# Kernel tuning notes

Measured on AMD Instinct MI355X. Metric: run time of the kernel, lower is better.

## Reference

```python
import jax, jax.numpy as jnp
import numpy as np

HEADS = 8
DIM_HEAD = 64
QUERY_DIM = 512
INNER = HEADS * DIM_HEAD
DIAG_OFFSET = 1
T_TEMP = 1.0
NEG_INF = -1e9  # used via -inf below; kept for clarity


def setup_inputs() -> dict:
    key = jax.random.key(0)
    ks = jax.random.split(key, 8)
    b, s, f = 2, 2048, 16
    x = jax.random.normal(ks[0], (b, s, f, QUERY_DIM), dtype=jnp.float32)
    pos_bias = jax.random.normal(ks[1], (HEADS, f, f), dtype=jnp.float32)
    w_scale = 0.02
    Wq = jax.random.normal(ks[2], (QUERY_DIM, INNER), dtype=jnp.float32) * w_scale
    Wk = jax.random.normal(ks[3], (QUERY_DIM, INNER), dtype=jnp.float32) * w_scale
    Wv = jax.random.normal(ks[4], (QUERY_DIM, INNER), dtype=jnp.float32) * w_scale
    Wo = jax.random.normal(ks[5], (INNER, QUERY_DIM), dtype=jnp.float32) * w_scale
    bo = jax.random.normal(ks[6], (QUERY_DIM,), dtype=jnp.float32) * w_scale
    return {"x": x, "pos_bias": pos_bias, "Wq": Wq, "Wk": Wk, "Wv": Wv, "Wo": Wo, "bo": bo}


def reference(x, pos_bias, Wq, Wk, Wv, Wo, bo):
    # x: [b, s, f, c] -- temporal attention over the frame axis f per spatial token
    b, s, f, _ = x.shape
    scale = DIM_HEAD ** -0.5
    q = (x @ Wq).reshape(b, s, f, HEADS, DIM_HEAD)
    k = (x @ Wk).reshape(b, s, f, HEADS, DIM_HEAD)
    v = (x @ Wv).reshape(b, s, f, HEADS, DIM_HEAD)
    # scores over frames: [b, s, h, f_q, f_k]
    w = jnp.einsum('bsihd,bsjhd->bshij', q * scale, k)
    w = w + pos_bias[None, None]  # [h, f, f] relative position bias
    # attend_prev_only causal mask (strict, diag_offset=1)
    causal = jnp.triu(jnp.ones((f, f), dtype=jnp.float32), k=DIAG_OFFSET)
    w = w + jnp.where(causal == 1.0, -jnp.inf, 0.0)
    # faithful to source: subtract row max, then softmax with temperature
    w = w - jax.lax.stop_gradient(jnp.max(w, axis=-1, keepdims=True))
    p = jax.nn.softmax(w.astype(jnp.float32) / T_TEMP, axis=-1).astype(w.dtype)
    out = jnp.einsum('bshij,bsjhd->bsihd', p, v).reshape(b, s, f, INNER)
    return out @ Wo + bo
```

## Files before the change

kernel.cpp:

```cpp
#include <hip/hip_runtime.h>

typedef unsigned short u16;
typedef __attribute__((ext_vector_type(8))) unsigned short u16x8;
typedef __attribute__((ext_vector_type(8))) __bf16 bf16x8;
typedef __attribute__((ext_vector_type(4))) float f32x4;

#define M_ROWS 65536
#define NQKV   1536
#define KDIM   512

typedef __attribute__((address_space(1))) const void gconst_void;
typedef __attribute__((address_space(3))) void lds_void;

static __device__ __forceinline__ u16 f2bf(float f) {
  unsigned u = __builtin_bit_cast(unsigned, f);
  u += 0x7FFFu + ((u >> 16) & 1u);
  return (u16)(u >> 16);
}

static __device__ __forceinline__ f32x4 mfma_bf16(u16x8 a, u16x8 b, f32x4 c) {
  return __builtin_amdgcn_mfma_f32_16x16x32_bf16(
      __builtin_bit_cast(bf16x8, a), __builtin_bit_cast(bf16x8, b), c, 0, 0, 0);
}

__global__ void conv_x(const float* __restrict__ x, u16* __restrict__ xb) {
  const size_t t = (size_t)blockIdx.x * 256 + threadIdx.x;
  f32x4 a = *(const f32x4*)(x + t * 8);
  f32x4 b = *(const f32x4*)(x + t * 8 + 4);
  u16x8 w;
#pragma unroll
  for (int e = 0; e < 4; ++e) { w[e] = f2bf(a[e]); w[e + 4] = f2bf(b[e]); }
  *(u16x8*)(xb + t * 8) = w;
}

__global__ void convW_qkv_t(const float* __restrict__ Wq, const float* __restrict__ Wk,
                            const float* __restrict__ Wv, u16* __restrict__ Wt) {
  __shared__ float tile[32][33];
  const int bn = blockIdx.x * 32;
  const int bk = blockIdx.y * 32;
  const int tx = threadIdx.x & 31, ty = threadIdx.x >> 5;
  const float* W = (bn < 512) ? Wq : ((bn < 1024) ? Wk : Wv);
  const int coln = bn & 511;
#pragma unroll
  for (int r = 0; r < 32; r += 8)
    tile[ty + r][tx] = W[(size_t)(bk + ty + r) * 512 + coln + tx];
  __syncthreads();
#pragma unroll
  for (int r = 0; r < 32; r += 8)
    Wt[(size_t)(bn + ty + r) * 512 + bk + tx] = f2bf(tile[tx][ty + r]);
}

__global__ void convWo_t(const float* __restrict__ Wo, u16* __restrict__ Wt) {
  __shared__ float tile[32][33];
  const int bn = blockIdx.x * 32;
  const int bk = blockIdx.y * 32;
  const int tx = threadIdx.x & 31, ty = threadIdx.x >> 5;
#pragma unroll
  for (int r = 0; r < 32; r += 8)
    tile[ty + r][tx] = Wo[(size_t)(bk + ty + r) * 512 + bn + tx];
  __syncthreads();
#pragma unroll
  for (int r = 0; r < 32; r += 8)
    Wt[(size_t)(bn + ty + r) * 512 + bk + tx] = f2bf(tile[tx][ty + r]);
}

__global__ __launch_bounds__(512, 2)
void gemm_qkv_attn(const u16* __restrict__ A, const u16* __restrict__ Wt,
                   const float* __restrict__ pos_bias, u16* __restrict__ attnbuf) {
  __shared__ __attribute__((aligned(16))) u16 smem[57344];
  u16* Ab   = smem;
  u16* Bb   = smem + 32768;
  u16* qkvT = smem;
  u16* Pl   = smem + 51200;

  const int tid  = threadIdx.x;
  const int lane = tid & 63;
  const int wid  = tid >> 6;
  const int wm   = wid >> 1;
  const int wn   = wid & 1;
  const int lg   = lane >> 4;
  const int lc   = lane & 15;
  const int srow = lane >> 3;
  const int sg   = (lane & 7) ^ srow;

  const int nwg  = gridDim.x;
  const int cpx  = nwg >> 3;
  const int flat = blockIdx.x;
  const int swz  = (flat & 7) * cpx + (flat >> 3);
  const int mt   = swz >> 3;
  const int h    = swz & 7;
  const int row0 = mt * 256;

  auto stagePh = [&](int ph, int b, int kt) {
    const int k0 = kt * 64;
    if (ph < 2) {
#pragma unroll
      for (int cc = 0; cc < 2; ++cc) {
        const int rl = wid * 32 + (ph * 2 + cc) * 8;
        const u16* src = A + (size_t)(row0 + rl + srow) * KDIM + k0 + sg * 8;
        __builtin_amdgcn_global_load_lds((gconst_void*)src,
                                         (lds_void*)&Ab[b * 16384 + rl * 64], 16, 0, 0);
      }
    } else {
      const int nj = (ph == 2) ? 2 : 1;
#pragma unroll
      for (int jj = 0; jj < 2; ++jj) {
        if (jj < nj) {
          const int j  = (ph == 2) ? jj : 2;
          const int rl = wid * 24 + j * 8;
          const int n  = rl + srow;
          const int grow = (n >> 6) * 512 + h * 64 + (n & 63);
          const u16* src = Wt + (size_t)grow * KDIM + k0 + sg * 8;
          __builtin_amdgcn_global_load_lds((gconst_void*)src,
                                           (lds_void*)&Bb[b * 12288 + rl * 64], 16, 0, 0);
        }
      }
    }
  };

  f32x4 acc[4][6];
#pragma unroll
  for (int mi = 0; mi < 4; ++mi)
#pragma unroll
    for (int ni = 0; ni < 6; ++ni) acc[mi][ni] = (f32x4){0.f, 0.f, 0.f, 0.f};

#pragma unroll
  for (int ph = 0; ph < 4; ++ph) stagePh(ph, 0, 0);
  asm volatile("s_waitcnt vmcnt(0)" ::: "memory");
  __builtin_amdgcn_s_barrier();

  for (int t = 0; t < 8; ++t) {
    const int  c   = t & 1;
    const bool pre = (t + 1) < 8;
    const u16* Asb = &Ab[c * 16384];
    const u16* Bsb = &Bb[c * 12288];
    u16x8 af[2], bfr[6];

#pragma unroll
    for (int ph = 0; ph < 4; ++ph) {
      const int ks = ph >> 1;
      const int mh = ph & 1;
      const int gsw = ((ks * 4 + lg) ^ (lc & 7)) << 3;
      if (mh == 0) {
#pragma unroll
        for (int ni = 0; ni < 6; ++ni)
          bfr[ni] = *(const u16x8*)&Bsb[(wn * 96 + ni * 16 + lc) * 64 + gsw];
      }
#pragma unroll
      for (int i = 0; i < 2; ++i)
        af[i] = *(const u16x8*)&Asb[(wm * 64 + (mh * 2 + i) * 16 + lc) * 64 + gsw];
      if (pre) stagePh(ph, c ^ 1, t + 1);

      __builtin_amdgcn_s_barrier();
      asm volatile("s_waitcnt lgkmcnt(0)" ::: "memory");
      __builtin_amdgcn_sched_barrier(0);
      __builtin_amdgcn_s_setprio(1);
#pragma unroll
      for (int i = 0; i < 2; ++i)
#pragma unroll
        for (int ni = 0; ni < 6; ++ni)
          acc[mh * 2 + i][ni] = mfma_bf16(af[i], bfr[ni], acc[mh * 2 + i][ni]);
      __builtin_amdgcn_s_setprio(0);
      __builtin_amdgcn_sched_barrier(0);
      if (ph < 3) __builtin_amdgcn_s_barrier();
    }
    asm volatile("s_waitcnt vmcnt(0)" ::: "memory");
    __builtin_amdgcn_s_barrier();
  }

#pragma unroll
  for (int mi = 0; mi < 4; ++mi)
#pragma unroll
    for (int ni = 0; ni < 6; ++ni) {
      const int col = wn * 96 + ni * 16 + lc;
      const int rb  = wm * 64 + mi * 16 + lg * 4;
#pragma unroll
      for (int r = 0; r < 4; ++r)
        qkvT[(rb + r) * 200 + col] = f2bf(acc[mi][ni][r]);
    }
  __syncthreads();

  const float scale = 0.125f;
  const f32x4 zf = {0.f, 0.f, 0.f, 0.f};
#pragma unroll
  for (int tt = 0; tt < 2; ++tt) {
    const int tok = wid * 2 + tt;
    const int rb  = tok * 16;
    const int qb  = (rb + lc) * 200;

    u16x8 aq0 = *(const u16x8*)&qkvT[qb + 0  + lg * 8];
    u16x8 aq1 = *(const u16x8*)&qkvT[qb + 32 + lg * 8];
    u16x8 bk0 = *(const u16x8*)&qkvT[qb + 64 + lg * 8];
    u16x8 bk1 = *(const u16x8*)&qkvT[qb + 96 + lg * 8];
    f32x4 s = mfma_bf16(aq0, bk0, zf);
    s = mfma_bf16(aq1, bk1, s);

    const int pb = wid * 512 + tt * 256;
#pragma unroll
    for (int r = 0; r < 4; ++r) {
      const int i = lg * 4 + r;
      float sv = s[r] * scale + pos_bias[h * 256 + i * 16 + lc];
      if (lc > i) sv = -1e30f;
      float m = sv;
#pragma unroll
      for (int off = 8; off >= 1; off >>= 1) m = fmaxf(m, __shfl_xor(m, off));
      float e = __expf(sv - m);
      float sm = e;
#pragma unroll
      for (int off = 8; off >= 1; off >>= 1) sm += __shfl_xor(sm, off);
      Pl[pb + i * 16 + lc] = f2bf(e / sm);
    }
    asm volatile("s_waitcnt lgkmcnt(0)" ::: "memory");

    u16x8 ap = {0, 0, 0, 0, 0, 0, 0, 0};
    if (lane < 32) ap = *(const u16x8*)&Pl[pb + lc * 16 + lg * 8];

#pragma unroll
    for (int nd = 0; nd < 4; ++nd) {
      u16x8 bv = {0, 0, 0, 0, 0, 0, 0, 0};
      if (lane < 32) {
#pragma unroll
        for (int jj = 0; jj < 8; ++jj) {
          const int j = lg * 8 + jj;
          bv[jj] = qkvT[(rb + j) * 200 + 128 + nd * 16 + lc];
        }
      }
      f32x4 o = mfma_bf16(ap, bv, zf);
#pragma unroll
      for (int r = 0; r < 4; ++r) {
        const int i = lg * 4 + r;
        attnbuf[(size_t)(row0 + rb + i) * 512 + h * 64 + nd * 16 + lc] = f2bf(o[r]);
      }
    }
  }
}

template <bool CF32>
__global__ __launch_bounds__(512, 2)
void gemm256(const u16* __restrict__ A, const u16* __restrict__ Bt,
             void* __restrict__ Cp, const float* __restrict__ bias,
             int N, int K, int n_tiles) {
  __shared__ __attribute__((aligned(16))) u16 smem[4][256 * 64];

  const int tid  = threadIdx.x;
  const int lane = tid & 63;
  const int wid  = tid >> 6;
  const int wm   = wid >> 2;
  const int wn   = wid & 3;
  const int lg   = lane >> 4;
  const int lc   = lane & 15;
  const int srow = lane >> 3;
  const int sg   = (lane & 7) ^ srow;

  const int nwg  = gridDim.x;
  const int cpx  = nwg >> 3;
  const int flat = blockIdx.x;
  const int swz  = (flat & 7) * cpx + (flat >> 3);
  const int mt   = swz / n_tiles;
  const int nt   = swz % n_tiles;
  const int row0 = mt * 256, col0 = nt * 256;

  auto stagePh = [&](int ph, int b, int kt) {
    const int k0 = kt * 64;
#pragma unroll
    for (int cc = 0; cc < 2; ++cc) {
      if (ph < 2) {
        const int c2 = ph * 2 + cc;
        const int rl = wid * 32 + c2 * 8;
        const u16* src = A + (size_t)(row0 + rl + srow) * K + k0 + sg * 8;
        __builtin_amdgcn_global_load_lds((gconst_void*)src,
                                         (lds_void*)&smem[b][rl * 64], 16, 0, 0);
      } else {
        const int c2 = (ph - 2) * 2 + cc;
        const int rl = wid * 32 + c2 * 8;
        const u16* src = Bt + (size_t)(col0 + rl + srow) * K + k0 + sg * 8;
        __builtin_amdgcn_global_load_lds((gconst_void*)src,
                                         (lds_void*)&smem[2 + b][rl * 64], 16, 0, 0);
      }
    }
  };

  f32x4 acc[8][4];
#pragma unroll
  for (int mi = 0; mi < 8; ++mi)
#pragma unroll
    for (int ni = 0; ni < 4; ++ni) acc[mi][ni] = (f32x4){0.f, 0.f, 0.f, 0.f};

  const int nkt = K >> 6;

#pragma unroll
  for (int ph = 0; ph < 4; ++ph) stagePh(ph, 0, 0);
  asm volatile("s_waitcnt vmcnt(0)" ::: "memory");
  __builtin_amdgcn_s_barrier();

  for (int t = 0; t < nkt; ++t) {
    const int  c   = t & 1;
    const bool pre = (t + 1) < nkt;
    const u16* Asb = &smem[c][0];
    const u16* Bsb = &smem[2 + c][0];
    u16x8 af[4], bfr[4];

#pragma unroll
    for (int ph = 0; ph < 4; ++ph) {
      const int ks = ph >> 1;
      const int mh = ph & 1;
      const int gsw = ((ks * 4 + lg) ^ (lc & 7)) << 3;
      if (mh == 0) {
#pragma unroll
        for (int ni = 0; ni < 4; ++ni)
          bfr[ni] = *(const u16x8*)&Bsb[(wn * 64 + ni * 16 + lc) * 64 + gsw];
      }
#pragma unroll
      for (int i = 0; i < 4; ++i)
        af[i] = *(const u16x8*)&Asb[(wm * 128 + (mh * 4 + i) * 16 + lc) * 64 + gsw];
      if (pre) stagePh(ph, c ^ 1, t + 1);

      __builtin_amdgcn_s_barrier();
      asm volatile("s_waitcnt lgkmcnt(0)" ::: "memory");
      __builtin_amdgcn_sched_barrier(0);
      __builtin_amdgcn_s_setprio(1);
#pragma unroll
      for (int i = 0; i < 4; ++i)
#pragma unroll
        for (int ni = 0; ni < 4; ++ni)
          acc[mh * 4 + i][ni] = mfma_bf16(af[i], bfr[ni], acc[mh * 4 + i][ni]);
      __builtin_amdgcn_s_setprio(0);
      __builtin_amdgcn_sched_barrier(0);
      if (ph < 3) __builtin_amdgcn_s_barrier();
    }
    asm volatile("s_waitcnt vmcnt(0)" ::: "memory");
    __builtin_amdgcn_s_barrier();
  }

  const int gmb = row0 + wm * 128;
  const int gnb = col0 + wn * 64;
#pragma unroll
  for (int mi = 0; mi < 8; ++mi)
#pragma unroll
    for (int ni = 0; ni < 4; ++ni) {
      const int gm = gmb + mi * 16 + lg * 4;
      const int gn = gnb + ni * 16 + lc;
      f32x4 v = acc[mi][ni];
      if constexpr (CF32) {
        float* C = (float*)Cp;
        float bv = bias[gn];
#pragma unroll
        for (int r = 0; r < 4; ++r) C[(size_t)(gm + r) * N + gn] = v[r] + bv;
      } else {
        u16* C = (u16*)Cp;
#pragma unroll
        for (int r = 0; r < 4; ++r) C[(size_t)(gm + r) * N + gn] = f2bf(v[r]);
      }
    }
}

extern "C" void kernel_launch(void* const* d_in, const int* in_sizes, int n_in,
                              void* d_out, int out_size, void* d_ws, size_t ws_size,
                              hipStream_t stream) {
  const float* x        = (const float*)d_in[0];
  const float* pos_bias = (const float*)d_in[1];
  const float* Wq       = (const float*)d_in[2];
  const float* Wk       = (const float*)d_in[3];
  const float* Wv       = (const float*)d_in[4];
  const float* Wo       = (const float*)d_in[5];
  const float* bo       = (const float*)d_in[6];
  float* out            = (float*)d_out;

  u16* xb      = (u16*)d_ws;
  u16* attnbuf = xb + (size_t)M_ROWS * 512;
  u16* Wo_t    = attnbuf + (size_t)M_ROWS * 512;
  u16* Wqkv_t  = (u16*)d_out;

  conv_x<<<dim3(M_ROWS * KDIM / (256 * 8)), dim3(256), 0, stream>>>(x, xb);

  convW_qkv_t<<<dim3(48, 16), dim3(256), 0, stream>>>(Wq, Wk, Wv, Wqkv_t);

  gemm_qkv_attn<<<dim3(2048), dim3(512), 0, stream>>>(xb, Wqkv_t, pos_bias, attnbuf);

  convWo_t<<<dim3(16, 16), dim3(256), 0, stream>>>(Wo, Wo_t);

  gemm256<true><<<dim3(512), dim3(512), 0, stream>>>(
      attnbuf, Wo_t, (void*)out, bo, 512, KDIM, 2);
}
```

Before: 225.1 us.

## Triple-buffer A tiles with two-ahead prefetch and retile output GEMM

Both GEMM kernels now keep three LDS buffers for the A operand and two for B. A is prefetched two k-steps ahead and B one ahead, and the end-of-iteration vmcnt(0) drain is replaced by a partial vmcnt(4) wait before each step. This is meant to overlap global-to-LDS loads with MFMA work instead of stalling at every k-step. The output projection is also retiled from 256x256 to 256x128 blocks, doubling the grid to 1024 workgroups. LDS use in the fused QKV kernel grows, and correctness now depends on the vmcnt counts matching the exact load issue order.

```diff
diff --git a/kernel.cpp b/kernel.cpp
--- a/kernel.cpp
+++ b/kernel.cpp
@@ -6,8 +6,8 @@
 typedef __attribute__((ext_vector_type(4))) float f32x4;
 
 #define M_ROWS 65536
-#define NQKV   1536
 #define KDIM   512
+#define NKT    8
 
 typedef __attribute__((address_space(1))) const void gconst_void;
 typedef __attribute__((address_space(3))) void lds_void;
@@ -67,9 +67,9 @@
 __global__ __launch_bounds__(512, 2)
 void gemm_qkv_attn(const u16* __restrict__ A, const u16* __restrict__ Wt,
                    const float* __restrict__ pos_bias, u16* __restrict__ attnbuf) {
-  __shared__ __attribute__((aligned(16))) u16 smem[57344];
+  __shared__ __attribute__((aligned(16))) u16 smem[73728];
   u16* Ab   = smem;
-  u16* Bb   = smem + 32768;
+  u16* Bb   = smem + 49152;
   u16* qkvT = smem;
   u16* Pl   = smem + 51200;
 
@@ -91,32 +91,19 @@
   const int h    = swz & 7;
   const int row0 = mt * 256;
 
-  auto stagePh = [&](int ph, int b, int kt) {
-    const int k0 = kt * 64;
-    if (ph < 2) {
-#pragma unroll
-      for (int cc = 0; cc < 2; ++cc) {
-        const int rl = wid * 32 + (ph * 2 + cc) * 8;
-        const u16* src = A + (size_t)(row0 + rl + srow) * KDIM + k0 + sg * 8;
-        __builtin_amdgcn_global_load_lds((gconst_void*)src,
-                                         (lds_void*)&Ab[b * 16384 + rl * 64], 16, 0, 0);
-      }
-    } else {
-      const int nj = (ph == 2) ? 2 : 1;
-#pragma unroll
-      for (int jj = 0; jj < 2; ++jj) {
-        if (jj < nj) {
-          const int j  = (ph == 2) ? jj : 2;
-          const int rl = wid * 24 + j * 8;
-          const int n  = rl + srow;
-          const int grow = (n >> 6) * 512 + h * 64 + (n & 63);
-          const u16* src = Wt + (size_t)grow * KDIM + k0 + sg * 8;
-          __builtin_amdgcn_global_load_lds((gconst_void*)src,
-                                           (lds_void*)&Bb[b * 12288 + rl * 64], 16, 0, 0);
-        }
-      }
-    }
+  auto stageA = [&](int buf, int unit, int kt) {
+    const int rl = unit * 64 + wid * 8;
+    const u16* src = A + (size_t)(row0 + rl + srow) * KDIM + kt * 64 + sg * 8;
+    __builtin_amdgcn_global_load_lds((gconst_void*)src,
+                                     (lds_void*)&Ab[buf * 16384 + rl * 64], 16, 0, 0);
   };
+  auto stageB = [&](int buf, int unit, int kt) {
+    const int rl = unit * 64 + wid * 8;
+    const int grow = unit * 512 + h * 64 + wid * 8 + srow;
+    const u16* src = Wt + (size_t)grow * KDIM + kt * 64 + sg * 8;
+    __builtin_amdgcn_global_load_lds((gconst_void*)src,
+                                     (lds_void*)&Bb[buf * 12288 + rl * 64], 16, 0, 0);
+  };
 
   f32x4 acc[4][6];
 #pragma unroll
@@ -125,17 +112,24 @@
     for (int ni = 0; ni < 6; ++ni) acc[mi][ni] = (f32x4){0.f, 0.f, 0.f, 0.f};
 
 #pragma unroll
-  for (int ph = 0; ph < 4; ++ph) stagePh(ph, 0, 0);
-  asm volatile("s_waitcnt vmcnt(0)" ::: "memory");
-  __builtin_amdgcn_s_barrier();
-
-  for (int t = 0; t < 8; ++t) {
-    const int  c   = t & 1;
-    const bool pre = (t + 1) < 8;
-    const u16* Asb = &Ab[c * 16384];
-    const u16* Bsb = &Bb[c * 12288];
+  for (int u = 0; u < 4; ++u) stageA(0, u, 0);
+#pragma unroll
+  for (int u = 0; u < 3; ++u) stageB(0, u, 0);
+#pragma unroll
+  for (int u = 0; u < 4; ++u) stageA(1, u, 1);
+
+  for (int t = 0; t < NKT; ++t) {
+    const int  ab   = t % 3;
+    const int  bb   = t & 1;
+    const bool preB = (t + 1) < NKT;
+    const bool preA = (t + 2) < NKT;
+    const int  ab2  = (t + 2) % 3;
+
+    if (t < NKT - 1) asm volatile("s_waitcnt vmcnt(4)" ::: "memory");
+    else             asm volatile("s_waitcnt vmcnt(0)" ::: "memory");
+    __builtin_amdgcn_s_barrier();
+
     u16x8 af[2], bfr[6];
-
 #pragma unroll
     for (int ph = 0; ph < 4; ++ph) {
       const int ks = ph >> 1;
@@ -144,12 +138,16 @@
       if (mh == 0) {
 #pragma unroll
         for (int ni = 0; ni < 6; ++ni)
-          bfr[ni] = *(const u16x8*)&Bsb[(wn * 96 + ni * 16 + lc) * 64 + gsw];
+          bfr[ni] = *(const u16x8*)&Bb[bb * 12288 + (wn * 96 + ni * 16 + lc) * 64 + gsw];
       }
 #pragma unroll
       for (int i = 0; i < 2; ++i)
-        af[i] = *(const u16x8*)&Asb[(wm * 64 + (mh * 2 + i) * 16 + lc) * 64 + gsw];
-      if (pre) stagePh(ph, c ^ 1, t + 1);
+        af[i] = *(const u16x8*)&Ab[ab * 16384 + (wm * 64 + (mh * 2 + i) * 16 + lc) * 64 + gsw];
+
+      if (ph == 0 && preB) { stageB(bb ^ 1, 0, t + 1); stageB(bb ^ 1, 1, t + 1); }
+      if (ph == 1) { if (preB) stageB(bb ^ 1, 2, t + 1); if (preA) stageA(ab2, 0, t + 2); }
+      if (ph == 2 && preA) { stageA(ab2, 1, t + 2); stageA(ab2, 2, t + 2); }
+      if (ph == 3 && preA) { stageA(ab2, 3, t + 2); }
 
       __builtin_amdgcn_s_barrier();
       asm volatile("s_waitcnt lgkmcnt(0)" ::: "memory");
@@ -164,9 +162,8 @@
       __builtin_amdgcn_sched_barrier(0);
       if (ph < 3) __builtin_amdgcn_s_barrier();
     }
-    asm volatile("s_waitcnt vmcnt(0)" ::: "memory");
-    __builtin_amdgcn_s_barrier();
   }
+  __syncthreads();
 
 #pragma unroll
   for (int mi = 0; mi < 4; ++mi)
@@ -235,18 +232,18 @@
   }
 }
 
-template <bool CF32>
 __global__ __launch_bounds__(512, 2)
-void gemm256(const u16* __restrict__ A, const u16* __restrict__ Bt,
-             void* __restrict__ Cp, const float* __restrict__ bias,
-             int N, int K, int n_tiles) {
-  __shared__ __attribute__((aligned(16))) u16 smem[4][256 * 64];
+void gemm_out(const u16* __restrict__ A, const u16* __restrict__ Bt,
+              float* __restrict__ C, const float* __restrict__ bias) {
+  __shared__ __attribute__((aligned(16))) u16 smem[65536];
+  u16* Ab = smem;
+  u16* Bb = smem + 49152;
 
   const int tid  = threadIdx.x;
   const int lane = tid & 63;
   const int wid  = tid >> 6;
-  const int wm   = wid >> 2;
-  const int wn   = wid & 3;
+  const int wm   = wid >> 1;
+  const int wn   = wid & 1;
   const int lg   = lane >> 4;
   const int lc   = lane & 15;
   const int srow = lane >> 3;
@@ -256,50 +253,48 @@
   const int cpx  = nwg >> 3;
   const int flat = blockIdx.x;
   const int swz  = (flat & 7) * cpx + (flat >> 3);
-  const int mt   = swz / n_tiles;
-  const int nt   = swz % n_tiles;
-  const int row0 = mt * 256, col0 = nt * 256;
-
-  auto stagePh = [&](int ph, int b, int kt) {
-    const int k0 = kt * 64;
-#pragma unroll
-    for (int cc = 0; cc < 2; ++cc) {
-      if (ph < 2) {
-        const int c2 = ph * 2 + cc;
-        const int rl = wid * 32 + c2 * 8;
-        const u16* src = A + (size_t)(row0 + rl + srow) * K + k0 + sg * 8;
-        __builtin_amdgcn_global_load_lds((gconst_void*)src,
-                                         (lds_void*)&smem[b][rl * 64], 16, 0, 0);
-      } else {
-        const int c2 = (ph - 2) * 2 + cc;
-        const int rl = wid * 32 + c2 * 8;
-        const u16* src = Bt + (size_t)(col0 + rl + srow) * K + k0 + sg * 8;
-        __builtin_amdgcn_global_load_lds((gconst_void*)src,
-                                         (lds_void*)&smem[2 + b][rl * 64], 16, 0, 0);
-      }
-    }
+  const int mt   = swz >> 2;
+  const int nt   = swz & 3;
+  const int row0 = mt * 256, col0 = nt * 128;
+
+  auto stageA = [&](int buf, int unit, int kt) {
+    const int rl = unit * 64 + wid * 8;
+    const u16* src = A + (size_t)(row0 + rl + srow) * KDIM + kt * 64 + sg * 8;
+    __builtin_amdgcn_global_load_lds((gconst_void*)src,
+                                     (lds_void*)&Ab[buf * 16384 + rl * 64], 16, 0, 0);
   };
-
-  f32x4 acc[8][4];
-#pragma unroll
-  for (int mi = 0; mi < 8; ++mi)
+  auto stageB = [&](int buf, int unit, int kt) {
+    const int rl = unit * 64 + wid * 8;
+    const u16* src = Bt + (size_t)(col0 + rl + srow) * KDIM + kt * 64 + sg * 8;
+    __builtin_amdgcn_global_load_lds((gconst_void*)src,
+                                     (lds_void*)&Bb[buf * 8192 + rl * 64], 16, 0, 0);
+  };
+
+  f32x4 acc[4][4];
+#pragma unroll
+  for (int mi = 0; mi < 4; ++mi)
 #pragma unroll
     for (int ni = 0; ni < 4; ++ni) acc[mi][ni] = (f32x4){0.f, 0.f, 0.f, 0.f};
 
-  const int nkt = K >> 6;
-
-#pragma unroll
-  for (int ph = 0; ph < 4; ++ph) stagePh(ph, 0, 0);
-  asm volatile("s_waitcnt vmcnt(0)" ::: "memory");
-  __builtin_amdgcn_s_barrier();
-
-  for (int t = 0; t < nkt; ++t) {
-    const int  c   = t & 1;
-    const bool pre = (t + 1) < nkt;
-    const u16* Asb = &smem[c][0];
-    const u16* Bsb = &smem[2 + c][0];
-    u16x8 af[4], bfr[4];
-
+#pragma unroll
+  for (int u = 0; u < 4; ++u) stageA(0, u, 0);
+#pragma unroll
+  for (int u = 0; u < 2; ++u) stageB(0, u, 0);
+#pragma unroll
+  for (int u = 0; u < 4; ++u) stageA(1, u, 1);
+
+  for (int t = 0; t < NKT; ++t) {
+    const int  ab   = t % 3;
+    const int  bb   = t & 1;
+    const bool preB = (t + 1) < NKT;
+    const bool preA = (t + 2) < NKT;
+    const int  ab2  = (t + 2) % 3;
+
+    if (t < NKT - 1) asm volatile("s_waitcnt vmcnt(4)" ::: "memory");
+    else             asm volatile("s_waitcnt vmcnt(0)" ::: "memory");
+    __builtin_amdgcn_s_barrier();
+
+    u16x8 af[2], bfr[4];
 #pragma unroll
     for (int ph = 0; ph < 4; ++ph) {
       const int ks = ph >> 1;
@@ -308,49 +303,43 @@
       if (mh == 0) {
 #pragma unroll
         for (int ni = 0; ni < 4; ++ni)
-          bfr[ni] = *(const u16x8*)&Bsb[(wn * 64 + ni * 16 + lc) * 64 + gsw];
+          bfr[ni] = *(const u16x8*)&Bb[bb * 8192 + (wn * 64 + ni * 16 + lc) * 64 + gsw];
       }
 #pragma unroll
-      for (int i = 0; i < 4; ++i)
-        af[i] = *(const u16x8*)&Asb[(wm * 128 + (mh * 4 + i) * 16 + lc) * 64 + gsw];
-      if (pre) stagePh(ph, c ^ 1, t + 1);
+      for (int i = 0; i < 2; ++i)
+        af[i] = *(const u16x8*)&Ab[ab * 16384 + (wm * 64 + (mh * 2 + i) * 16 + lc) * 64 + gsw];
+
+      if (ph == 0 && preB) { stageB(bb ^ 1, 0, t + 1); stageB(bb ^ 1, 1, t + 1); }
+      if (ph == 1 && preA) { stageA(ab2, 0, t + 2); stageA(ab2, 1, t + 2); }
+      if (ph == 2 && preA) { stageA(ab2, 2, t + 2); stageA(ab2, 3, t + 2); }
 
       __builtin_amdgcn_s_barrier();
       asm volatile("s_waitcnt lgkmcnt(0)" ::: "memory");
       __builtin_amdgcn_sched_barrier(0);
       __builtin_amdgcn_s_setprio(1);
 #pragma unroll
-      for (int i = 0; i < 4; ++i)
+      for (int i = 0; i < 2; ++i)
 #pragma unroll
         for (int ni = 0; ni < 4; ++ni)
-          acc[mh * 4 + i][ni] = mfma_bf16(af[i], bfr[ni], acc[mh * 4 + i][ni]);
+          acc[mh * 2 + i][ni] = mfma_bf16(af[i], bfr[ni], acc[mh * 2 + i][ni]);
       __builtin_amdgcn_s_setprio(0);
       __builtin_amdgcn_sched_barrier(0);
       if (ph < 3) __builtin_amdgcn_s_barrier();
     }
-    asm volatile("s_waitcnt vmcnt(0)" ::: "memory");
-    __builtin_amdgcn_s_barrier();
   }
 
-  const int gmb = row0 + wm * 128;
+  const int gmb = row0 + wm * 64;
   const int gnb = col0 + wn * 64;
 #pragma unroll
-  for (int mi = 0; mi < 8; ++mi)
+  for (int mi = 0; mi < 4; ++mi)
 #pragma unroll
     for (int ni = 0; ni < 4; ++ni) {
       const int gm = gmb + mi * 16 + lg * 4;
       const int gn = gnb + ni * 16 + lc;
+      const float bv = bias[gn];
       f32x4 v = acc[mi][ni];
-      if constexpr (CF32) {
-        float* C = (float*)Cp;
-        float bv = bias[gn];
-#pragma unroll
-        for (int r = 0; r < 4; ++r) C[(size_t)(gm + r) * N + gn] = v[r] + bv;
-      } else {
-        u16* C = (u16*)Cp;
-#pragma unroll
-        for (int r = 0; r < 4; ++r) C[(size_t)(gm + r) * N + gn] = f2bf(v[r]);
-      }
+#pragma unroll
+      for (int r = 0; r < 4; ++r) C[(size_t)(gm + r) * 512 + gn] = v[r] + bv;
     }
 }
 
@@ -372,13 +361,8 @@
   u16* Wqkv_t  = (u16*)d_out;
 
   conv_x<<<dim3(M_ROWS * KDIM / (256 * 8)), dim3(256), 0, stream>>>(x, xb);
-
   convW_qkv_t<<<dim3(48, 16), dim3(256), 0, stream>>>(Wq, Wk, Wv, Wqkv_t);
-
   gemm_qkv_attn<<<dim3(2048), dim3(512), 0, stream>>>(xb, Wqkv_t, pos_bias, attnbuf);
-
   convWo_t<<<dim3(16, 16), dim3(256), 0, stream>>>(Wo, Wo_t);
-
-  gemm256<true><<<dim3(512), dim3(512), 0, stream>>>(
-      attnbuf, Wo_t, (void*)out, bo, 512, KDIM, 2);
-}
+  gemm_out<<<dim3(1024), dim3(512), 0, stream>>>(attnbuf, Wo_t, out, bo);
+}
```

Result: no change. 224.3 us (-0.4%).
